# Kernel tuning notes

Measured on AMD Instinct MI355X. Metric: run time of the kernel, lower is better.

The kernel has to match this reference:

```python
import jax, jax.numpy as jnp
import numpy as np

B, N, D = 8, 1024, 768
H, Z = 12, 64          # num_heads, head_dim (D = H*Z)
HID = 3072             # int(D * mlp_ratio)


def setup_inputs() -> dict:
    key = jax.random.key(0)
    k1, k2, k3, k4 = jax.random.split(key, 4)
    s = 0.02
    x = jax.random.normal(k1, (B, N, D), dtype=jnp.float32)
    Wq = jax.random.normal(k2, (D, D), dtype=jnp.float32) * s
    Wk = jax.random.normal(k3, (D, D), dtype=jnp.float32) * s
    betas = jnp.full((H,), Z ** -0.5, dtype=jnp.float32)
    W_mlp = jax.random.normal(k4, (HID, D), dtype=jnp.float32) * s
    return {"x": x, "Wq": Wq, "Wk": Wk, "betas": betas, "W_mlp": W_mlp}


def reference(x, Wq, Wk, betas, W_mlp):
    # --- KQ-aligned attention ---
    # torch Linear: y = x @ W.T ; weight shape [out=D, in=D]
    Q = jnp.einsum('bnd,ed->bne', x, Wq).reshape(B, N, H, Z).transpose(0, 2, 1, 3)  # bhqz
    K = jnp.einsum('bnd,ed->bne', x, Wk).reshape(B, N, H, Z).transpose(0, 2, 1, 3)  # bhkz
    Wq_r = Wq.reshape(H, Z, D)
    Wk_r = Wk.reshape(H, Z, D)
    F1 = jnp.einsum('hzd,bhkz->bkhd', Wq_r, K)
    F2 = jnp.einsum('hzd,bhqz->bqhd', Wk_r, Q)
    scores = jnp.einsum('bhqz,bhkz,h->bhqk', Q, K, betas)
    attn = jax.nn.softmax(scores, axis=-1)
    T1 = jnp.einsum('bkhd,bhqk->bqd', F1, attn)
    T2 = jnp.einsum('bqhd,bhqk->bkd', F2, attn)
    # --- symmetric-weight Hopfield MLP (bias=False) ---
    hid = jax.nn.relu(jnp.einsum('bnd,hd->bnh', x, W_mlp))
    mlp = jnp.einsum('bnh,hd->bnd', hid, W_mlp)
    return T1 + T2 + mlp
```

## Files before the change

kernel.cpp:

```cpp
#include <hip/hip_runtime.h>
#include <hip/hip_bf16.h>

#define Bq 8
#define Nq 1024
#define Dq 768
#define Hq 12
#define Zq 64
#define HIDq 3072
#define BN (Bq*Nq)
#define QKP 1536

typedef unsigned short u16;
typedef short s16x8 __attribute__((ext_vector_type(8)));
typedef float f32x4 __attribute__((ext_vector_type(4)));
typedef unsigned short u16x4 __attribute__((ext_vector_type(4)));

#define MFMA16 __builtin_amdgcn_mfma_f32_16x16x32_bf16
#define GLOAD16(g, l) __builtin_amdgcn_global_load_lds( \
    (const __attribute__((address_space(1))) void*)(const void*)(g), \
    (__attribute__((address_space(3))) void*)(l), 16, 0, 0)

__device__ __forceinline__ u16 f2bf(float f) {
  unsigned u = __float_as_uint(f);
  return (u16)((u + 0x7FFFu + ((u >> 16) & 1u)) >> 16);
}

__device__ __forceinline__ void xcd_swizzle(int gx, int gy, int& bx, int& by) {
  int l = blockIdx.y * gx + blockIdx.x;
  int c = l & 7, j = l >> 3;
  by = c * (gy >> 3) + j / gx;
  bx = j % gx;
}

__global__ __launch_bounds__(256) void cvt_bf16(const float* __restrict__ in,
                                                u16* __restrict__ out, int n) {
  int i = (blockIdx.x * 256 + threadIdx.x) * 4;
  if (i >= n) return;
  float4 v = *(const float4*)&in[i];
  u16x4 o; o[0] = f2bf(v.x); o[1] = f2bf(v.y); o[2] = f2bf(v.z); o[3] = f2bf(v.w);
  *(u16x4*)&out[i] = o;
}

__global__ __launch_bounds__(256) void cvt_tr(const float* __restrict__ in,
                                              u16* __restrict__ out, u16* __restrict__ outT,
                                              int C, int out_p, int outT_p) {
  __shared__ u16 T[64][72];
  const int t = threadIdx.x;
  const int r0 = blockIdx.y * 64, c0 = blockIdx.x * 64;
  const int r = t >> 3, c8 = (t & 7) * 8;
#pragma unroll
  for (int p = 0; p < 2; p++) {
    const float* ip = &in[(size_t)(r0 + r + p * 32) * C + c0 + c8];
    float4 v0 = *(const float4*)ip, v1 = *(const float4*)(ip + 4);
    u16 tmp[8] = {f2bf(v0.x), f2bf(v0.y), f2bf(v0.z), f2bf(v0.w),
                  f2bf(v1.x), f2bf(v1.y), f2bf(v1.z), f2bf(v1.w)};
    *(uint4*)&out[(size_t)(r0 + r + p * 32) * out_p + c0 + c8] = *(uint4*)tmp;
    *(uint4*)&T[r + p * 32][c8] = *(uint4*)tmp;
  }
  __syncthreads();
#pragma unroll
  for (int p = 0; p < 2; p++) {
    int oc = r + p * 32;
    u16 tmp[8];
#pragma unroll
    for (int j = 0; j < 8; j++) tmp[j] = T[c8 + j][oc];
    *(uint4*)&outT[(size_t)(c0 + oc) * outT_p + r0 + c8] = *(uint4*)tmp;
  }
}

__global__ __launch_bounds__(256) void transpose_bf16(
    const u16* __restrict__ in, u16* __restrict__ out,
    int in_pitch, int out_pitch, int inner_n,
    long in_bs_o, long in_bs_i, long out_bs_o, long out_bs_i) {
  __shared__ u16 T[64][72];
  const int t = threadIdx.x;
  const int bz = blockIdx.z;
  const long iboff = (long)(bz / inner_n) * in_bs_o + (long)(bz % inner_n) * in_bs_i;
  const long oboff = (long)(bz / inner_n) * out_bs_o + (long)(bz % inner_n) * out_bs_i;
  const u16* ip = in + iboff + (long)(blockIdx.y * 64) * in_pitch + blockIdx.x * 64;
  u16* op = out + oboff + (long)(blockIdx.x * 64) * out_pitch + blockIdx.y * 64;
  const int r = t >> 3, c8 = (t & 7) * 8;
#pragma unroll
  for (int p = 0; p < 2; p++)
    *(uint4*)&T[r + p * 32][c8] = *(const uint4*)(ip + (size_t)(r + p * 32) * in_pitch + c8);
  __syncthreads();
#pragma unroll
  for (int p = 0; p < 2; p++) {
    int oc = r + p * 32;
    u16 tmp[8];
#pragma unroll
    for (int j = 0; j < 8; j++) tmp[j] = T[c8 + j][oc];
    *(uint4*)(op + (size_t)oc * out_pitch + c8) = *(uint4*)tmp;
  }
}

template<bool RELU>
__global__ __launch_bounds__(256) void gemm_bf16(
    const u16* __restrict__ A, const u16* __restrict__ B, u16* __restrict__ C,
    int M, int N, int K) {
  __shared__ u16 As[128 * 32];
  __shared__ u16 Bs[128 * 32];
  int bx, by;
  xcd_swizzle(gridDim.x, gridDim.y, bx, by);
  const int t = threadIdx.x, l = t & 63, w = t >> 6;
  const int lq = l & 15, quad = l >> 4;
  const int bm = by * 128, bn = bx * 128;
  const int wm = (w & 1) * 64, wn = (w >> 1) * 64;
  f32x4 acc[4][4];
#pragma unroll
  for (int i = 0; i < 4; i++)
#pragma unroll
    for (int j = 0; j < 4; j++) acc[i][j] = (f32x4){0.f, 0.f, 0.f, 0.f};

  for (int k0 = 0; k0 < K; k0 += 32) {
#pragma unroll
    for (int p = 0; p < 2; p++) {
      int idx = p * 256 + t;
      GLOAD16(A + (size_t)(bm + (idx >> 2)) * K + k0 + (idx & 3) * 8, As + idx * 8);
      GLOAD16(B + (size_t)(bn + (idx >> 2)) * K + k0 + (idx & 3) * 8, Bs + idx * 8);
    }
    __syncthreads();
    s16x8 af[4], bf[4];
#pragma unroll
    for (int mt = 0; mt < 4; mt++) af[mt] = *(const s16x8*)&As[(wm + mt * 16 + lq) * 32 + quad * 8];
#pragma unroll
    for (int nt = 0; nt < 4; nt++) bf[nt] = *(const s16x8*)&Bs[(wn + nt * 16 + lq) * 32 + quad * 8];
#pragma unroll
    for (int mt = 0; mt < 4; mt++)
#pragma unroll
      for (int nt = 0; nt < 4; nt++)
        acc[mt][nt] = MFMA16(af[mt], bf[nt], acc[mt][nt], 0, 0, 0);
    __syncthreads();
  }
#pragma unroll
  for (int mt = 0; mt < 4; mt++)
#pragma unroll
    for (int nt = 0; nt < 4; nt++) {
      int row = bm + wm + mt * 16 + quad * 4;
      int col = bn + wn + nt * 16 + lq;
#pragma unroll
      for (int r = 0; r < 4; r++) {
        float v = acc[mt][nt][r];
        if (RELU) v = fmaxf(v, 0.f);
        C[(size_t)(row + r) * N + col] = f2bf(v);
      }
    }
}

__global__ __launch_bounds__(256) void gemm_out2(
    const u16* __restrict__ AV12, const u16* __restrict__ hid,
    const u16* __restrict__ WqkT, const u16* __restrict__ WmT,
    float* __restrict__ out) {
  __shared__ u16 As[128 * 32];
  __shared__ u16 Bs[64 * 32];
  int bx, by;
  xcd_swizzle(gridDim.x, gridDim.y, bx, by);
  const int t = threadIdx.x, l = t & 63, w = t >> 6;
  const int lq = l & 15, quad = l >> 4;
  const int bm = by * 128, bn = bx * 64;
  const int wm = w * 32;
  f32x4 acc[2][4];
#pragma unroll
  for (int i = 0; i < 2; i++)
#pragma unroll
    for (int j = 0; j < 4; j++) acc[i][j] = (f32x4){0.f, 0.f, 0.f, 0.f};

#pragma unroll
  for (int src = 0; src < 2; src++) {
    const u16* A = src ? hid : AV12;
    const u16* B = src ? WmT : WqkT;
    const int pitch = src ? HIDq : QKP;
    const int Kend = src ? HIDq : QKP;
    for (int k0 = 0; k0 < Kend; k0 += 32) {
#pragma unroll
      for (int p = 0; p < 2; p++) {
        int idx = p * 256 + t;
        GLOAD16(A + (size_t)(bm + (idx >> 2)) * pitch + k0 + (idx & 3) * 8, As + idx * 8);
      }
      GLOAD16(B + (size_t)(bn + (t >> 2)) * pitch + k0 + (t & 3) * 8, Bs + t * 8);
      __syncthreads();
      s16x8 af[2], bf[4];
#pragma unroll
      for (int mt = 0; mt < 2; mt++)
        af[mt] = *(const s16x8*)&As[(wm + mt * 16 + lq) * 32 + quad * 8];
#pragma unroll
      for (int nt = 0; nt < 4; nt++)
        bf[nt] = *(const s16x8*)&Bs[(nt * 16 + lq) * 32 + quad * 8];
#pragma unroll
      for (int mt = 0; mt < 2; mt++)
#pragma unroll
        for (int nt = 0; nt < 4; nt++)
          acc[mt][nt] = MFMA16(af[mt], bf[nt], acc[mt][nt], 0, 0, 0);
      __syncthreads();
    }
  }
#pragma unroll
  for (int mt = 0; mt < 2; mt++)
#pragma unroll
    for (int nt = 0; nt < 4; nt++) {
      int row = bm + wm + mt * 16 + quad * 4;
      int col = bn + nt * 16 + lq;
#pragma unroll
      for (int r = 0; r < 4; r++)
        out[(size_t)(row + r) * Dq + col] = acc[mt][nt][r];
    }
}

__global__ __launch_bounds__(256) void attn_pass1(
    const u16* __restrict__ QKb, const u16* __restrict__ KbT,
    const float* __restrict__ betas, u16* __restrict__ AV12,
    float* __restrict__ lg) {
  __shared__ u16 Qs[2][64][32];
  __shared__ u16 Ks[2][64][32];
  __shared__ u16 Kts[2][64][32];
  __shared__ u16 Ps[64][72];
  __shared__ float red[4][64];
  __shared__ float li[64];

  const int t = threadIdx.x, l = t & 63, w = t >> 6;
  const int lq = l & 15, quad = l >> 4;
  const int c = blockIdx.x & 7, j = blockIdx.x >> 3;
  const int bh = c * 12 + j / 16, qt = j % 16;
  const int b = bh / Hq, h = bh % Hq;
  const int q0 = qt * 64;
  const float beta = betas[h];
  const u16* Qh = QKb + (size_t)(b * Nq) * QKP + h * 64;
  const u16* Kh = Qh + Dq;
  const u16* KTh = KbT + (size_t)bh * 64 * Nq;
  u16* QsF = &Qs[0][0][0]; u16* KsF = &Ks[0][0][0]; u16* KtsF = &Kts[0][0][0];

#pragma unroll
  for (int p = 0; p < 2; p++) {
    int idx = p * 256 + t;
    GLOAD16(Qh + (size_t)(q0 + ((idx >> 2) & 63)) * QKP + (idx >> 8) * 32 + (idx & 3) * 8,
            QsF + idx * 8);
  }
  __syncthreads();
  s16x8 bqf[2][4];
#pragma unroll
  for (int zs = 0; zs < 2; zs++)
#pragma unroll
    for (int nt = 0; nt < 4; nt++)
      bqf[zs][nt] = *(const s16x8*)&Qs[zs][nt * 16 + lq][quad * 8];

  float lsum[4] = {0.f, 0.f, 0.f, 0.f};
  f32x4 ao[4];
#pragma unroll
  for (int nt = 0; nt < 4; nt++) ao[nt] = (f32x4){0.f, 0.f, 0.f, 0.f};

  for (int kt = 0; kt < 16; kt++) {
#pragma unroll
    for (int p = 0; p < 2; p++) {
      int idx = p * 256 + t;
      GLOAD16(Kh + (size_t)(kt * 64 + ((idx >> 2) & 63)) * QKP + (idx >> 8) * 32 + (idx & 3) * 8,
              KsF + idx * 8);
      GLOAD16(KTh + (size_t)((idx >> 2) & 63) * Nq + kt * 64 + (idx >> 8) * 32 + (idx & 3) * 8,
              KtsF + idx * 8);
    }
    __syncthreads();
    f32x4 sc[4];
#pragma unroll
    for (int nt = 0; nt < 4; nt++) sc[nt] = (f32x4){0.f, 0.f, 0.f, 0.f};
#pragma unroll
    for (int zs = 0; zs < 2; zs++) {
      s16x8 a = *(const s16x8*)&Ks[zs][w * 16 + lq][quad * 8];
#pragma unroll
      for (int nt = 0; nt < 4; nt++)
        sc[nt] = MFMA16(a, bqf[zs][nt], sc[nt], 0, 0, 0);
    }
#pragma unroll
    for (int nt = 0; nt < 4; nt++) {
      u16x4 pk;
#pragma unroll
      for (int r = 0; r < 4; r++) {
        float e = __expf(sc[nt][r] * beta);
        lsum[nt] += e;
        pk[r] = f2bf(e);
      }
      *(u16x4*)&Ps[nt * 16 + lq][w * 16 + quad * 4] = pk;
    }
    __syncthreads();
#pragma unroll
    for (int ks = 0; ks < 2; ks++) {
      s16x8 a = *(const s16x8*)&Ps[w * 16 + lq][ks * 32 + quad * 8];
#pragma unroll
      for (int nt = 0; nt < 4; nt++) {
        s16x8 bk = *(const s16x8*)&Kts[ks][nt * 16 + lq][quad * 8];
        ao[nt] = MFMA16(a, bk, ao[nt], 0, 0, 0);
      }
    }
    __syncthreads();
  }
#pragma unroll
  for (int nt = 0; nt < 4; nt++) {
    float v = lsum[nt];
    v += __shfl_xor(v, 16, 64);
    v += __shfl_xor(v, 32, 64);
    if (l < 16) red[w][nt * 16 + lq] = v;
  }
  __syncthreads();
  if (t < 64) {
    float s = red[0][t] + red[1][t] + red[2][t] + red[3][t];
    lg[(size_t)bh * Nq + q0 + t] = s;
    li[t] = 1.0f / s;
  }
  __syncthreads();
  u16* Oh = AV12 + (size_t)(b * Nq + q0) * QKP + h * 64;
  float lr[4];
#pragma unroll
  for (int r = 0; r < 4; r++) lr[r] = li[w * 16 + quad * 4 + r];
#pragma unroll
  for (int nt = 0; nt < 4; nt++)
#pragma unroll
    for (int r = 0; r < 4; r++)
      Oh[(size_t)(w * 16 + quad * 4 + r) * QKP + nt * 16 + lq] = f2bf(ao[nt][r] * lr[r]);
}

__global__ __launch_bounds__(256) void attn_pass2(
    const u16* __restrict__ QKb, const u16* __restrict__ QbT,
    const float* __restrict__ betas, u16* __restrict__ AV12,
    const float* __restrict__ lg) {
  __shared__ u16 Qs[2][64][32];
  __shared__ u16 Qts[2][64][32];
  __shared__ u16 Ks[2][64][32];
  __shared__ u16 Pts[64][72];
  __shared__ float li_s[64];

  const int t = threadIdx.x, l = t & 63, w = t >> 6;
  const int lq = l & 15, quad = l >> 4;
  const int c = blockIdx.x & 7, j = blockIdx.x >> 3;
  const int bh = c * 12 + j / 16, kt = j % 16;
  const int b = bh / Hq, h = bh % Hq;
  const int k0 = kt * 64;
  const float beta = betas[h];
  const u16* Qh = QKb + (size_t)(b * Nq) * QKP + h * 64;
  const u16* Kh = Qh + Dq;
  const u16* QTh = QbT + (size_t)bh * 64 * Nq;
  u16* QsF = &Qs[0][0][0]; u16* QtsF = &Qts[0][0][0]; u16* KsF = &Ks[0][0][0];

#pragma unroll
  for (int p = 0; p < 2; p++) {
    int idx = p * 256 + t;
    GLOAD16(Kh + (size_t)(k0 + ((idx >> 2) & 63)) * QKP + (idx >> 8) * 32 + (idx & 3) * 8,
            KsF + idx * 8);
  }
  __syncthreads();
  s16x8 bkf[2][4];
#pragma unroll
  for (int zs = 0; zs < 2; zs++)
#pragma unroll
    for (int nt = 0; nt < 4; nt++)
      bkf[zs][nt] = *(const s16x8*)&Ks[zs][nt * 16 + lq][quad * 8];

  f32x4 ao[4];
#pragma unroll
  for (int nt = 0; nt < 4; nt++) ao[nt] = (f32x4){0.f, 0.f, 0.f, 0.f};

  for (int qt = 0; qt < 16; qt++) {
#pragma unroll
    for (int p = 0; p < 2; p++) {
      int idx = p * 256 + t;
      GLOAD16(Qh + (size_t)(qt * 64 + ((idx >> 2) & 63)) * QKP + (idx >> 8) * 32 + (idx & 3) * 8,
              QsF + idx * 8);
      GLOAD16(QTh + (size_t)((idx >> 2) & 63) * Nq + qt * 64 + (idx >> 8) * 32 + (idx & 3) * 8,
              QtsF + idx * 8);
    }
    if (t < 64) li_s[t] = 1.0f / lg[(size_t)bh * Nq + qt * 64 + t];
    __syncthreads();
    f32x4 sc[4];
#pragma unroll
    for (int nt = 0; nt < 4; nt++) sc[nt] = (f32x4){0.f, 0.f, 0.f, 0.f};
#pragma unroll
    for (int zs = 0; zs < 2; zs++) {
      s16x8 a = *(const s16x8*)&Qs[zs][w * 16 + lq][quad * 8];
#pragma unroll
      for (int nt = 0; nt < 4; nt++)
        sc[nt] = MFMA16(a, bkf[zs][nt], sc[nt], 0, 0, 0);
    }
    float lr[4];
#pragma unroll
    for (int r = 0; r < 4; r++) lr[r] = li_s[w * 16 + quad * 4 + r];
#pragma unroll
    for (int nt = 0; nt < 4; nt++) {
      u16x4 pk;
#pragma unroll
      for (int r = 0; r < 4; r++)
        pk[r] = f2bf(__expf(sc[nt][r] * beta) * lr[r]);
      *(u16x4*)&Pts[nt * 16 + lq][w * 16 + quad * 4] = pk;
    }
    __syncthreads();
#pragma unroll
    for (int qs = 0; qs < 2; qs++) {
      s16x8 a = *(const s16x8*)&Pts[w * 16 + lq][qs * 32 + quad * 8];
#pragma unroll
      for (int nt = 0; nt < 4; nt++) {
        s16x8 bq = *(const s16x8*)&Qts[qs][nt * 16 + lq][quad * 8];
        ao[nt] = MFMA16(a, bq, ao[nt], 0, 0, 0);
      }
    }
    __syncthreads();
  }
  u16* Oh = AV12 + (size_t)(b * Nq + k0) * QKP + Dq + h * 64;
#pragma unroll
  for (int nt = 0; nt < 4; nt++)
#pragma unroll
    for (int r = 0; r < 4; r++)
      Oh[(size_t)(w * 16 + quad * 4 + r) * QKP + nt * 16 + lq] = f2bf(ao[nt][r]);
}

extern "C" void kernel_launch(void* const* d_in, const int* in_sizes, int n_in,
                              void* d_out, int out_size, void* d_ws, size_t ws_size,
                              hipStream_t stream) {
  const float* x     = (const float*)d_in[0];
  const float* Wq    = (const float*)d_in[1];
  const float* Wk    = (const float*)d_in[2];
  const float* betas = (const float*)d_in[3];
  const float* Wm    = (const float*)d_in[4];
  float* out = (float*)d_out;

  u16* xb   = (u16*)d_ws;
  u16* Wqkb = xb + (size_t)BN * Dq;
  u16* Wmb  = Wqkb + (size_t)QKP * Dq;
  u16* WqkT = Wmb + (size_t)HIDq * Dq;
  u16* QKb  = WqkT + (size_t)Dq * QKP;
  u16* QbT  = QKb + (size_t)BN * QKP;
  u16* KbT  = QbT + (size_t)Bq * Hq * Zq * Nq;
  u16* AV12 = KbT + (size_t)Bq * Hq * Zq * Nq;
  float* lg = (float*)(AV12 + (size_t)BN * QKP);
  u16* hidb = QKb;
  u16* WmT  = xb;

  dim3 blk(256);
  cvt_bf16<<<(BN * Dq) / 1024, blk, 0, stream>>>(x, xb, BN * Dq);
  cvt_tr<<<dim3(12, 12), blk, 0, stream>>>(Wq, Wqkb, WqkT, Dq, Dq, QKP);
  cvt_tr<<<dim3(12, 12), blk, 0, stream>>>(Wk, Wqkb + (size_t)Dq * Dq, WqkT + Dq, Dq, Dq, QKP);
  cvt_bf16<<<(HIDq * Dq) / 1024, blk, 0, stream>>>(Wm, Wmb, HIDq * Dq);

  gemm_bf16<false><<<dim3(QKP / 128, BN / 128), blk, 0, stream>>>(
      xb, Wqkb, QKb, BN, QKP, Dq);

  transpose_bf16<<<dim3(1, 16, 96), blk, 0, stream>>>(QKb, QbT, QKP, Nq, Hq,
      (long)Nq * QKP, 64, (long)Hq * 64 * Nq, (long)64 * Nq);
  transpose_bf16<<<dim3(1, 16, 96), blk, 0, stream>>>(QKb + Dq, KbT, QKP, Nq, Hq,
      (long)Nq * QKP, 64, (long)Hq * 64 * Nq, (long)64 * Nq);

  attn_pass1<<<Bq * Hq * 16, blk, 0, stream>>>(QKb, KbT, betas, AV12, lg);
  attn_pass2<<<Bq * Hq * 16, blk, 0, stream>>>(QKb, QbT, betas, AV12, lg);

  gemm_bf16<true><<<dim3(HIDq / 128, BN / 128), blk, 0, stream>>>(
      xb, Wmb, hidb, BN, HIDq, Dq);

  transpose_bf16<<<dim3(12, 48, 1), blk, 0, stream>>>(Wmb, WmT, Dq, HIDq, 1, 0, 0, 0, 0);

  gemm_out2<<<dim3(Dq / 64, BN / 128), blk, 0, stream>>>(AV12, hidb, WqkT, WmT, out);
}
```

Baseline: 388.2 us.

## Replace GEMMs with single-wave 64x64 tiles using 32x32x16 MFMA

Replaces the 256-thread 128x128 and 128x64 GEMM kernels with one templated single-wavefront kernel. Each block computes a 64x64 tile with 32x32x16 bf16 MFMAs and stages operands in LDS already laid out in fragment order. The kernel serves the QK projection, the ReLU MLP up-projection and the dual-source output GEMM. The aim is more blocks and fewer LDS reads per MFMA, at the cost of less operand reuse per block, more global traffic, and a sync per k-step with no double buffering.

```diff
diff --git a/kernel.cpp b/kernel.cpp
--- a/kernel.cpp
+++ b/kernel.cpp
@@ -13,9 +13,11 @@
 typedef unsigned short u16;
 typedef short s16x8 __attribute__((ext_vector_type(8)));
 typedef float f32x4 __attribute__((ext_vector_type(4)));
+typedef float f32x16 __attribute__((ext_vector_type(16)));
 typedef unsigned short u16x4 __attribute__((ext_vector_type(4)));
 
 #define MFMA16 __builtin_amdgcn_mfma_f32_16x16x32_bf16
+#define MFMA32 __builtin_amdgcn_mfma_f32_32x32x16_bf16
 #define GLOAD16(g, l) __builtin_amdgcn_global_load_lds( \
     (const __attribute__((address_space(1))) void*)(const void*)(g), \
     (__attribute__((address_space(3))) void*)(l), 16, 0, 0)
@@ -94,116 +96,72 @@
   }
 }
 
-template<bool RELU>
-__global__ __launch_bounds__(256) void gemm_bf16(
-    const u16* __restrict__ A, const u16* __restrict__ B, u16* __restrict__ C,
-    int M, int N, int K) {
-  __shared__ u16 As[128 * 32];
-  __shared__ u16 Bs[128 * 32];
+template<bool RELU, bool DUAL, bool OUTF32>
+__global__ __launch_bounds__(64, 4) void gemm_w64(
+    const u16* __restrict__ A0, const u16* __restrict__ B0, int pitch0, int K0,
+    const u16* __restrict__ A1, const u16* __restrict__ B1, int pitch1, int K1,
+    void* __restrict__ Cv, int N) {
+  __shared__ u16 As[2048];
+  __shared__ u16 Bs[2048];
   int bx, by;
   xcd_swizzle(gridDim.x, gridDim.y, bx, by);
-  const int t = threadIdx.x, l = t & 63, w = t >> 6;
-  const int lq = l & 15, quad = l >> 4;
-  const int bm = by * 128, bn = bx * 128;
-  const int wm = (w & 1) * 64, wn = (w >> 1) * 64;
-  f32x4 acc[4][4];
-#pragma unroll
-  for (int i = 0; i < 4; i++)
-#pragma unroll
-    for (int j = 0; j < 4; j++) acc[i][j] = (f32x4){0.f, 0.f, 0.f, 0.f};
-
-  for (int k0 = 0; k0 < K; k0 += 32) {
-#pragma unroll
-    for (int p = 0; p < 2; p++) {
-      int idx = p * 256 + t;
-      GLOAD16(A + (size_t)(bm + (idx >> 2)) * K + k0 + (idx & 3) * 8, As + idx * 8);
-      GLOAD16(B + (size_t)(bn + (idx >> 2)) * K + k0 + (idx & 3) * 8, Bs + idx * 8);
-    }
-    __syncthreads();
-    s16x8 af[4], bf[4];
-#pragma unroll
-    for (int mt = 0; mt < 4; mt++) af[mt] = *(const s16x8*)&As[(wm + mt * 16 + lq) * 32 + quad * 8];
-#pragma unroll
-    for (int nt = 0; nt < 4; nt++) bf[nt] = *(const s16x8*)&Bs[(wn + nt * 16 + lq) * 32 + quad * 8];
-#pragma unroll
-    for (int mt = 0; mt < 4; mt++)
-#pragma unroll
-      for (int nt = 0; nt < 4; nt++)
-        acc[mt][nt] = MFMA16(af[mt], bf[nt], acc[mt][nt], 0, 0, 0);
-    __syncthreads();
-  }
-#pragma unroll
-  for (int mt = 0; mt < 4; mt++)
-#pragma unroll
-    for (int nt = 0; nt < 4; nt++) {
-      int row = bm + wm + mt * 16 + quad * 4;
-      int col = bn + wn + nt * 16 + lq;
-#pragma unroll
-      for (int r = 0; r < 4; r++) {
+  const int l = threadIdx.x;
+  const int ln = l & 31, kh = l >> 5;
+  const int bm = by * 64, bn = bx * 64;
+
+  f32x16 acc[2][2];
+#pragma unroll
+  for (int i = 0; i < 2; i++)
+#pragma unroll
+    for (int j = 0; j < 2; j++)
+#pragma unroll
+      for (int r = 0; r < 16; r++) acc[i][j][r] = 0.f;
+
+  const int nsrc = DUAL ? 2 : 1;
+  for (int s = 0; s < nsrc; s++) {
+    const u16* A = s ? A1 : A0;
+    const u16* B = s ? B1 : B0;
+    const int pitch = s ? pitch1 : pitch0;
+    const int Kend = s ? K1 : K0;
+    for (int k0 = 0; k0 < Kend; k0 += 32) {
+#pragma unroll
+      for (int ks = 0; ks < 2; ks++)
+#pragma unroll
+        for (int m = 0; m < 2; m++) {
+          const int ch = (ks * 2 + m) * 512;
+          GLOAD16(A + (size_t)(bm + m * 32 + ln) * pitch + k0 + ks * 16 + kh * 8,
+                  As + ch + l * 8);
+          GLOAD16(B + (size_t)(bn + m * 32 + ln) * pitch + k0 + ks * 16 + kh * 8,
+                  Bs + ch + l * 8);
+        }
+      __syncthreads();
+#pragma unroll
+      for (int ks = 0; ks < 2; ks++) {
+        s16x8 a0 = *(const s16x8*)&As[(ks * 2 + 0) * 512 + l * 8];
+        s16x8 a1 = *(const s16x8*)&As[(ks * 2 + 1) * 512 + l * 8];
+        s16x8 b0 = *(const s16x8*)&Bs[(ks * 2 + 0) * 512 + l * 8];
+        s16x8 b1 = *(const s16x8*)&Bs[(ks * 2 + 1) * 512 + l * 8];
+        acc[0][0] = MFMA32(a0, b0, acc[0][0], 0, 0, 0);
+        acc[0][1] = MFMA32(a0, b1, acc[0][1], 0, 0, 0);
+        acc[1][0] = MFMA32(a1, b0, acc[1][0], 0, 0, 0);
+        acc[1][1] = MFMA32(a1, b1, acc[1][1], 0, 0, 0);
+      }
+      __syncthreads();
+    }
+  }
+#pragma unroll
+  for (int mt = 0; mt < 2; mt++)
+#pragma unroll
+    for (int nt = 0; nt < 2; nt++)
+#pragma unroll
+      for (int r = 0; r < 16; r++) {
+        int row = bm + mt * 32 + (r & 3) + 8 * (r >> 2) + 4 * kh;
+        int col = bn + nt * 32 + ln;
         float v = acc[mt][nt][r];
         if (RELU) v = fmaxf(v, 0.f);
-        C[(size_t)(row + r) * N + col] = f2bf(v);
+        if (OUTF32) ((float*)Cv)[(size_t)row * N + col] = v;
+        else        ((u16*)Cv)[(size_t)row * N + col] = f2bf(v);
       }
-    }
-}
-
-__global__ __launch_bounds__(256) void gemm_out2(
-    const u16* __restrict__ AV12, const u16* __restrict__ hid,
-    const u16* __restrict__ WqkT, const u16* __restrict__ WmT,
-    float* __restrict__ out) {
-  __shared__ u16 As[128 * 32];
-  __shared__ u16 Bs[64 * 32];
-  int bx, by;
-  xcd_swizzle(gridDim.x, gridDim.y, bx, by);
-  const int t = threadIdx.x, l = t & 63, w = t >> 6;
-  const int lq = l & 15, quad = l >> 4;
-  const int bm = by * 128, bn = bx * 64;
-  const int wm = w * 32;
-  f32x4 acc[2][4];
-#pragma unroll
-  for (int i = 0; i < 2; i++)
-#pragma unroll
-    for (int j = 0; j < 4; j++) acc[i][j] = (f32x4){0.f, 0.f, 0.f, 0.f};
-
-#pragma unroll
-  for (int src = 0; src < 2; src++) {
-    const u16* A = src ? hid : AV12;
-    const u16* B = src ? WmT : WqkT;
-    const int pitch = src ? HIDq : QKP;
-    const int Kend = src ? HIDq : QKP;
-    for (int k0 = 0; k0 < Kend; k0 += 32) {
-#pragma unroll
-      for (int p = 0; p < 2; p++) {
-        int idx = p * 256 + t;
-        GLOAD16(A + (size_t)(bm + (idx >> 2)) * pitch + k0 + (idx & 3) * 8, As + idx * 8);
-      }
-      GLOAD16(B + (size_t)(bn + (t >> 2)) * pitch + k0 + (t & 3) * 8, Bs + t * 8);
-      __syncthreads();
-      s16x8 af[2], bf[4];
-#pragma unroll
-      for (int mt = 0; mt < 2; mt++)
-        af[mt] = *(const s16x8*)&As[(wm + mt * 16 + lq) * 32 + quad * 8];
-#pragma unroll
-      for (int nt = 0; nt < 4; nt++)
-        bf[nt] = *(const s16x8*)&Bs[(nt * 16 + lq) * 32 + quad * 8];
-#pragma unroll
-      for (int mt = 0; mt < 2; mt++)
-#pragma unroll
-        for (int nt = 0; nt < 4; nt++)
-          acc[mt][nt] = MFMA16(af[mt], bf[nt], acc[mt][nt], 0, 0, 0);
-      __syncthreads();
-    }
-  }
-#pragma unroll
-  for (int mt = 0; mt < 2; mt++)
-#pragma unroll
-    for (int nt = 0; nt < 4; nt++) {
-      int row = bm + wm + mt * 16 + quad * 4;
-      int col = bn + nt * 16 + lq;
-#pragma unroll
-      for (int r = 0; r < 4; r++)
-        out[(size_t)(row + r) * Dq + col] = acc[mt][nt][r];
-    }
 }
 
 __global__ __launch_bounds__(256) void attn_pass1(
@@ -436,8 +394,8 @@
   cvt_tr<<<dim3(12, 12), blk, 0, stream>>>(Wk, Wqkb + (size_t)Dq * Dq, WqkT + Dq, Dq, Dq, QKP);
   cvt_bf16<<<(HIDq * Dq) / 1024, blk, 0, stream>>>(Wm, Wmb, HIDq * Dq);
 
-  gemm_bf16<false><<<dim3(QKP / 128, BN / 128), blk, 0, stream>>>(
-      xb, Wqkb, QKb, BN, QKP, Dq);
+  gemm_w64<false, false, false><<<dim3(QKP / 64, BN / 64), dim3(64), 0, stream>>>(
+      xb, Wqkb, Dq, Dq, nullptr, nullptr, 0, 0, QKb, QKP);
 
   transpose_bf16<<<dim3(1, 16, 96), blk, 0, stream>>>(QKb, QbT, QKP, Nq, Hq,
       (long)Nq * QKP, 64, (long)Hq * 64 * Nq, (long)64 * Nq);
@@ -447,10 +405,11 @@
   attn_pass1<<<Bq * Hq * 16, blk, 0, stream>>>(QKb, KbT, betas, AV12, lg);
   attn_pass2<<<Bq * Hq * 16, blk, 0, stream>>>(QKb, QbT, betas, AV12, lg);
 
-  gemm_bf16<true><<<dim3(HIDq / 128, BN / 128), blk, 0, stream>>>(
-      xb, Wmb, hidb, BN, HIDq, Dq);
+  gemm_w64<true, false, false><<<dim3(HIDq / 64, BN / 64), dim3(64), 0, stream>>>(
+      xb, Wmb, Dq, Dq, nullptr, nullptr, 0, 0, hidb, HIDq);
 
   transpose_bf16<<<dim3(12, 48, 1), blk, 0, stream>>>(Wmb, WmT, Dq, HIDq, 1, 0, 0, 0, 0);
 
-  gemm_out2<<<dim3(Dq / 64, BN / 128), blk, 0, stream>>>(AV12, hidb, WqkT, WmT, out);
-}
+  gemm_w64<false, true, true><<<dim3(Dq / 64, BN / 64), dim3(64), 0, stream>>>(
+      AV12, WqkT, QKP, QKP, hidb, WmT, HIDq, HIDq, out, Dq);
+}
```

New measurement: 663.9 us. 1.71x slower.

## Load GEMM B-operand fragments directly from global into registers with prefetch

Applied to the files above, without the earlier changes.

Both GEMM kernels stop staging the B tile through LDS. Each lane now loads its B fragments straight from global memory into registers, prefetching the next k-step while the current MFMAs run. This removes the LDS writes and reads for B and halves LDS use. In exchange, the B loads become per-lane 16-byte reads spread across 16 rows, which are less coalesced. Each B element is also reread by every wave that shares the same columns instead of being shared through LDS, and register pressure rises.

```diff
diff --git a/kernel.cpp b/kernel.cpp
--- a/kernel.cpp
+++ b/kernel.cpp
@@ -99,7 +99,6 @@
     const u16* __restrict__ A, const u16* __restrict__ B, u16* __restrict__ C,
     int M, int N, int K) {
   __shared__ u16 As[128 * 32];
-  __shared__ u16 Bs[128 * 32];
   int bx, by;
   xcd_swizzle(gridDim.x, gridDim.y, bx, by);
   const int t = threadIdx.x, l = t & 63, w = t >> 6;
@@ -112,24 +111,38 @@
 #pragma unroll
     for (int j = 0; j < 4; j++) acc[i][j] = (f32x4){0.f, 0.f, 0.f, 0.f};
 
+  const u16* Bp[4];
+#pragma unroll
+  for (int nt = 0; nt < 4; nt++)
+    Bp[nt] = B + (size_t)(bn + wn + nt * 16 + lq) * K + quad * 8;
+  s16x8 bf_cur[4], bf_nxt[4];
+#pragma unroll
+  for (int nt = 0; nt < 4; nt++) bf_cur[nt] = *(const s16x8*)Bp[nt];
+
   for (int k0 = 0; k0 < K; k0 += 32) {
 #pragma unroll
     for (int p = 0; p < 2; p++) {
       int idx = p * 256 + t;
       GLOAD16(A + (size_t)(bm + (idx >> 2)) * K + k0 + (idx & 3) * 8, As + idx * 8);
-      GLOAD16(B + (size_t)(bn + (idx >> 2)) * K + k0 + (idx & 3) * 8, Bs + idx * 8);
-    }
-    __syncthreads();
-    s16x8 af[4], bf[4];
+    }
+    const bool more = (k0 + 32) < K;
+    if (more) {
+#pragma unroll
+      for (int nt = 0; nt < 4; nt++) bf_nxt[nt] = *(const s16x8*)(Bp[nt] + k0 + 32);
+    }
+    __syncthreads();
+    s16x8 af[4];
 #pragma unroll
     for (int mt = 0; mt < 4; mt++) af[mt] = *(const s16x8*)&As[(wm + mt * 16 + lq) * 32 + quad * 8];
 #pragma unroll
-    for (int nt = 0; nt < 4; nt++) bf[nt] = *(const s16x8*)&Bs[(wn + nt * 16 + lq) * 32 + quad * 8];
-#pragma unroll
     for (int mt = 0; mt < 4; mt++)
 #pragma unroll
       for (int nt = 0; nt < 4; nt++)
-        acc[mt][nt] = MFMA16(af[mt], bf[nt], acc[mt][nt], 0, 0, 0);
+        acc[mt][nt] = MFMA16(af[mt], bf_cur[nt], acc[mt][nt], 0, 0, 0);
+    if (more) {
+#pragma unroll
+      for (int nt = 0; nt < 4; nt++) bf_cur[nt] = bf_nxt[nt];
+    }
     __syncthreads();
   }
 #pragma unroll
@@ -152,7 +165,6 @@
     const u16* __restrict__ WqkT, const u16* __restrict__ WmT,
     float* __restrict__ out) {
   __shared__ u16 As[128 * 32];
-  __shared__ u16 Bs[64 * 32];
   int bx, by;
   xcd_swizzle(gridDim.x, gridDim.y, bx, by);
   const int t = threadIdx.x, l = t & 63, w = t >> 6;
@@ -171,26 +183,39 @@
     const u16* B = src ? WmT : WqkT;
     const int pitch = src ? HIDq : QKP;
     const int Kend = src ? HIDq : QKP;
+    const u16* Bp[4];
+#pragma unroll
+    for (int nt = 0; nt < 4; nt++)
+      Bp[nt] = B + (size_t)(bn + nt * 16 + lq) * pitch + quad * 8;
+    s16x8 bf_cur[4], bf_nxt[4];
+#pragma unroll
+    for (int nt = 0; nt < 4; nt++) bf_cur[nt] = *(const s16x8*)Bp[nt];
+
     for (int k0 = 0; k0 < Kend; k0 += 32) {
 #pragma unroll
       for (int p = 0; p < 2; p++) {
         int idx = p * 256 + t;
         GLOAD16(A + (size_t)(bm + (idx >> 2)) * pitch + k0 + (idx & 3) * 8, As + idx * 8);
       }
-      GLOAD16(B + (size_t)(bn + (t >> 2)) * pitch + k0 + (t & 3) * 8, Bs + t * 8);
+      const bool more = (k0 + 32) < Kend;
+      if (more) {
+#pragma unroll
+        for (int nt = 0; nt < 4; nt++) bf_nxt[nt] = *(const s16x8*)(Bp[nt] + k0 + 32);
+      }
       __syncthreads();
-      s16x8 af[2], bf[4];
+      s16x8 af[2];
 #pragma unroll
       for (int mt = 0; mt < 2; mt++)
         af[mt] = *(const s16x8*)&As[(wm + mt * 16 + lq) * 32 + quad * 8];
 #pragma unroll
-      for (int nt = 0; nt < 4; nt++)
-        bf[nt] = *(const s16x8*)&Bs[(nt * 16 + lq) * 32 + quad * 8];
-#pragma unroll
       for (int mt = 0; mt < 2; mt++)
 #pragma unroll
         for (int nt = 0; nt < 4; nt++)
-          acc[mt][nt] = MFMA16(af[mt], bf[nt], acc[mt][nt], 0, 0, 0);
+          acc[mt][nt] = MFMA16(af[mt], bf_cur[nt], acc[mt][nt], 0, 0, 0);
+      if (more) {
+#pragma unroll
+        for (int nt = 0; nt < 4; nt++) bf_cur[nt] = bf_nxt[nt];
+      }
       __syncthreads();
     }
   }
```

Result: slower. 585.6 us (+50.9%).

## Double-buffer LDS tiles in GEMM kernels and widen output GEMM K-tile

Applied to the files above, without the earlier changes.

Both the generic bf16 GEMM and the fused output GEMM now keep two LDS buffers. The next K-slice is issued with async global-to-LDS loads while MFMAs run on the current slice, and only one barrier is used per iteration. The output GEMM also doubles its K step to 64, walking both the attention and MLP sources as one 72-tile loop. The aim is to hide global-load latency and cut barrier overhead, at the cost of twice the LDS per block, which may lower occupancy.

```diff
diff --git a/kernel.cpp b/kernel.cpp
--- a/kernel.cpp
+++ b/kernel.cpp
@@ -98,8 +98,8 @@
 __global__ __launch_bounds__(256) void gemm_bf16(
     const u16* __restrict__ A, const u16* __restrict__ B, u16* __restrict__ C,
     int M, int N, int K) {
-  __shared__ u16 As[128 * 32];
-  __shared__ u16 Bs[128 * 32];
+  __shared__ u16 As[2][128 * 32];
+  __shared__ u16 Bs[2][128 * 32];
   int bx, by;
   xcd_swizzle(gridDim.x, gridDim.y, bx, by);
   const int t = threadIdx.x, l = t & 63, w = t >> 6;
@@ -112,25 +112,32 @@
 #pragma unroll
     for (int j = 0; j < 4; j++) acc[i][j] = (f32x4){0.f, 0.f, 0.f, 0.f};
 
-  for (int k0 = 0; k0 < K; k0 += 32) {
+  auto stage = [&](int k0, int bufi) {
 #pragma unroll
     for (int p = 0; p < 2; p++) {
       int idx = p * 256 + t;
-      GLOAD16(A + (size_t)(bm + (idx >> 2)) * K + k0 + (idx & 3) * 8, As + idx * 8);
-      GLOAD16(B + (size_t)(bn + (idx >> 2)) * K + k0 + (idx & 3) * 8, Bs + idx * 8);
-    }
-    __syncthreads();
+      GLOAD16(A + (size_t)(bm + (idx >> 2)) * K + k0 + (idx & 3) * 8, &As[bufi][idx * 8]);
+      GLOAD16(B + (size_t)(bn + (idx >> 2)) * K + k0 + (idx & 3) * 8, &Bs[bufi][idx * 8]);
+    }
+  };
+  stage(0, 0);
+  const int nIter = K >> 5;
+  for (int it = 0; it < nIter; it++) {
+    __syncthreads();
+    if (it + 1 < nIter) stage((it + 1) * 32, (it + 1) & 1);
+    const int bi = it & 1;
     s16x8 af[4], bf[4];
 #pragma unroll
-    for (int mt = 0; mt < 4; mt++) af[mt] = *(const s16x8*)&As[(wm + mt * 16 + lq) * 32 + quad * 8];
-#pragma unroll
-    for (int nt = 0; nt < 4; nt++) bf[nt] = *(const s16x8*)&Bs[(wn + nt * 16 + lq) * 32 + quad * 8];
+    for (int mt = 0; mt < 4; mt++)
+      af[mt] = *(const s16x8*)&As[bi][(wm + mt * 16 + lq) * 32 + quad * 8];
+#pragma unroll
+    for (int nt = 0; nt < 4; nt++)
+      bf[nt] = *(const s16x8*)&Bs[bi][(wn + nt * 16 + lq) * 32 + quad * 8];
 #pragma unroll
     for (int mt = 0; mt < 4; mt++)
 #pragma unroll
       for (int nt = 0; nt < 4; nt++)
         acc[mt][nt] = MFMA16(af[mt], bf[nt], acc[mt][nt], 0, 0, 0);
-    __syncthreads();
   }
 #pragma unroll
   for (int mt = 0; mt < 4; mt++)
@@ -151,8 +158,8 @@
     const u16* __restrict__ AV12, const u16* __restrict__ hid,
     const u16* __restrict__ WqkT, const u16* __restrict__ WmT,
     float* __restrict__ out) {
-  __shared__ u16 As[128 * 32];
-  __shared__ u16 Bs[64 * 32];
+  __shared__ u16 As[2][128 * 64];
+  __shared__ u16 Bs[2][64 * 64];
   int bx, by;
   xcd_swizzle(gridDim.x, gridDim.y, bx, by);
   const int t = threadIdx.x, l = t & 63, w = t >> 6;
@@ -165,33 +172,42 @@
 #pragma unroll
     for (int j = 0; j < 4; j++) acc[i][j] = (f32x4){0.f, 0.f, 0.f, 0.f};
 
-#pragma unroll
-  for (int src = 0; src < 2; src++) {
-    const u16* A = src ? hid : AV12;
-    const u16* B = src ? WmT : WqkT;
-    const int pitch = src ? HIDq : QKP;
-    const int Kend = src ? HIDq : QKP;
-    for (int k0 = 0; k0 < Kend; k0 += 32) {
-#pragma unroll
-      for (int p = 0; p < 2; p++) {
-        int idx = p * 256 + t;
-        GLOAD16(A + (size_t)(bm + (idx >> 2)) * pitch + k0 + (idx & 3) * 8, As + idx * 8);
-      }
-      GLOAD16(B + (size_t)(bn + (t >> 2)) * pitch + k0 + (t & 3) * 8, Bs + t * 8);
-      __syncthreads();
+  auto stage = [&](int tl, int bufi) {
+    const u16* A; const u16* B; int pitch, k0;
+    if (tl < 24) { A = AV12; B = WqkT; pitch = QKP;  k0 = tl * 64; }
+    else         { A = hid;  B = WmT;  pitch = HIDq; k0 = (tl - 24) * 64; }
+#pragma unroll
+    for (int p = 0; p < 4; p++) {
+      int idx = p * 256 + t, ks = idx >> 9, rem = idx & 511;
+      GLOAD16(A + (size_t)(bm + (rem >> 2)) * pitch + k0 + ks * 32 + (rem & 3) * 8,
+              &As[bufi][idx * 8]);
+    }
+#pragma unroll
+    for (int p = 0; p < 2; p++) {
+      int idx = p * 256 + t, ks = idx >> 8, rem = idx & 255;
+      GLOAD16(B + (size_t)(bn + (rem >> 2)) * pitch + k0 + ks * 32 + (rem & 3) * 8,
+              &Bs[bufi][idx * 8]);
+    }
+  };
+  stage(0, 0);
+  for (int tl = 0; tl < 72; tl++) {
+    __syncthreads();
+    if (tl + 1 < 72) stage(tl + 1, (tl + 1) & 1);
+    const int bi = tl & 1;
+#pragma unroll
+    for (int ks = 0; ks < 2; ks++) {
       s16x8 af[2], bf[4];
 #pragma unroll
       for (int mt = 0; mt < 2; mt++)
-        af[mt] = *(const s16x8*)&As[(wm + mt * 16 + lq) * 32 + quad * 8];
+        af[mt] = *(const s16x8*)&As[bi][ks * 4096 + (wm + mt * 16 + lq) * 32 + quad * 8];
 #pragma unroll
       for (int nt = 0; nt < 4; nt++)
-        bf[nt] = *(const s16x8*)&Bs[(nt * 16 + lq) * 32 + quad * 8];
+        bf[nt] = *(const s16x8*)&Bs[bi][ks * 2048 + (nt * 16 + lq) * 32 + quad * 8];
 #pragma unroll
       for (int mt = 0; mt < 2; mt++)
 #pragma unroll
         for (int nt = 0; nt < 4; nt++)
           acc[mt][nt] = MFMA16(af[mt], bf[nt], acc[mt][nt], 0, 0, 0);
-      __syncthreads();
     }
   }
 #pragma unroll
```

Measured after the change: 364.8 us. 6.0% less time.
